# Performance work log

Measured on AMD Instinct MI355X. Metric: run time of the kernel, lower is better.

## Reference

```python
import jax, jax.numpy as jnp
import numpy as np

EMB, HEADS = 1024, 16
HD = EMB // HEADS


def setup_inputs() -> dict:
    key = jax.random.key(0)
    ks = jax.random.split(key, 9)
    B, T, C = 4, 2048, EMB
    s = 1.0 / np.sqrt(C)
    return {
        "x": jax.random.normal(ks[0], (B, T, C), jnp.float32),
        "Wq": jax.random.normal(ks[1], (C, C), jnp.float32) * s,
        "bq": jnp.zeros((C,), jnp.float32),
        "Wk": jax.random.normal(ks[2], (C, C), jnp.float32) * s,
        "bk": jnp.zeros((C,), jnp.float32),
        "Wv": jax.random.normal(ks[3], (C, C), jnp.float32) * s,
        "bv": jnp.zeros((C,), jnp.float32),
        "Wo": jax.random.normal(ks[4], (C, C), jnp.float32) * s,
        "bo": jnp.zeros((C,), jnp.float32),
    }


def _attn(x, Wq, bq, Wk, bk, Wv, bv, Wo, bo):
    B, T, C = x.shape
    # [B,T,C] -> [B,H,T,hd]
    def split(h):
        return h.reshape(B, T, HEADS, HD).transpose(0, 2, 1, 3)
    q = split(x @ Wq + bq)
    k = split(x @ Wk + bk)
    v = split(x @ Wv + bv)
    att = jnp.einsum("bhtd,bhsd->bhts", q, k) * (1.0 / np.sqrt(HD))
    causal = jnp.tril(jnp.ones((T, T), bool))  # [T,T]
    att = jnp.where(causal, att, -jnp.inf)
    att = jax.nn.softmax(att, axis=-1)
    y = jnp.einsum("bhts,bhsd->bhtd", att, v)
    y = y.transpose(0, 2, 1, 3).reshape(B, T, C)
    return y @ Wo + bo


def reference(x, Wq, bq, Wk, bk, Wv, bv, Wo, bo):
    return _attn(x, Wq, bq, Wk, bk, Wv, bv, Wo, bo)
```

## Files before the change

### kernel.cpp

```cpp
#include <hip/hip_runtime.h>
#include <cmath>

#define EMB 1024
#define HEADS 16
#define HD 64
#define BATCH 4
#define SEQ 2048
#define MTOT (BATCH * SEQ)

typedef __attribute__((ext_vector_type(8))) short short8;
typedef __attribute__((ext_vector_type(4))) float f32x4;
typedef __attribute__((ext_vector_type(16))) float f32x16;

__device__ __forceinline__ float b2f(unsigned short u) {
  union { unsigned int i; float f; } c; c.i = ((unsigned int)u) << 16; return c.f;
}
__device__ __forceinline__ unsigned short f2b(float f) {
  union { float f; unsigned int i; } c; c.f = f;
  unsigned int x = c.i;
  return (unsigned short)((x + 0x7fffu + ((x >> 16) & 1u)) >> 16);
}

#define GLD16(gp, lp) __builtin_amdgcn_global_load_lds( \
    (__attribute__((address_space(1))) unsigned int*)(gp), \
    (__attribute__((address_space(3))) unsigned int*)(lp), 16, 0, 0)

__global__ __launch_bounds__(256) void prep(
    const float* __restrict__ x, unsigned short* __restrict__ xb,
    const float* __restrict__ W0, const float* __restrict__ W1,
    const float* __restrict__ W2, const float* __restrict__ W3,
    unsigned short* __restrict__ Wt) {
  const int b = blockIdx.x;
  if (b < 4096) {
    const size_t i = ((size_t)b * 256 + threadIdx.x) * 8;
    const float4 a = *(const float4*)(x + i);
    const float4 c = *(const float4*)(x + i + 4);
    ushort4 lo = {f2b(a.x), f2b(a.y), f2b(a.z), f2b(a.w)};
    ushort4 hi = {f2b(c.x), f2b(c.y), f2b(c.z), f2b(c.w)};
    *(ushort4*)(xb + i) = lo;
    *(ushort4*)(xb + i + 4) = hi;
  } else {
    __shared__ float T[32][33];
    const int bb = b - 4096;
    const int z = bb >> 10;
    const float* W = (z == 0) ? W0 : (z == 1) ? W1 : (z == 2) ? W2 : W3;
    unsigned short* out = Wt + (size_t)z * EMB * EMB;
    const int k0 = (bb & 31) * 32, n0 = ((bb >> 5) & 31) * 32;
    const int tx = threadIdx.x & 31, ty = threadIdx.x >> 5;
#pragma unroll
    for (int r = 0; r < 4; ++r)
      T[ty + r * 8][tx] = W[(size_t)(k0 + ty + r * 8) * EMB + n0 + tx];
    __syncthreads();
#pragma unroll
    for (int r = 0; r < 4; ++r)
      out[(size_t)(n0 + ty + r * 8) * EMB + k0 + tx] = f2b(T[tx][ty + r * 8]);
  }
}

#define GEMM_STAGE64(Asrc_, Bsrc_, kb_)                                     \
  do {                                                                      \
    _Pragma("unroll")                                                       \
    for (int j_ = 0; j_ < 4; ++j_) {                                        \
      const int t_ = w * 4 + j_;                                            \
      const int r_ = t_ * 8 + r8;                                           \
      GLD16((Asrc_) + (size_t)(row0 + r_) * EMB + (kb_) + c8x,              \
            &As[t_ * 512]);                                                 \
      GLD16((Bsrc_) + (size_t)(col0 + r_) * EMB + (kb_) + c8x,              \
            &Bs[t_ * 512]);                                                 \
    }                                                                       \
  } while (0)

#define GEMM_KLOOP64(Asrc_, Bsrc_)                                          \
  const int r8 = lane >> 3;                                                 \
  const int c8x = ((lane & 7) ^ r8) * 8;                                    \
  for (int kb = 0; kb < EMB; kb += 64) {                                    \
    if (kb) __syncthreads();                                                \
    GEMM_STAGE64(Asrc_, Bsrc_, kb);                                         \
    __syncthreads();                                                        \
    _Pragma("unroll")                                                       \
    for (int kc = 0; kc < 2; ++kc) {                                        \
      short8 af[4], bf[4];                                                  \
      _Pragma("unroll")                                                     \
      for (int i = 0; i < 4; ++i)                                           \
        af[i] = *(const short8*)                                            \
            &As[(wm + i * 16 + m) * 64 + (((kc * 4 + g) ^ (m & 7)) * 8)];   \
      _Pragma("unroll")                                                     \
      for (int j = 0; j < 4; ++j)                                           \
        bf[j] = *(const short8*)                                            \
            &Bs[(wn + j * 16 + m) * 64 + (((kc * 4 + g) ^ (m & 7)) * 8)];   \
      _Pragma("unroll")                                                     \
      for (int i = 0; i < 4; ++i)                                           \
        _Pragma("unroll")                                                   \
        for (int j = 0; j < 4; ++j)                                         \
          acc[i][j] = __builtin_amdgcn_mfma_f32_16x16x32_bf16(              \
              af[i], bf[j], acc[i][j], 0, 0, 0);                            \
    }                                                                       \
  }

template <int OUTMODE>
__global__ __launch_bounds__(256) void gemm_mfma(
    const unsigned short* __restrict__ A, const unsigned short* __restrict__ Bt,
    const float* __restrict__ bias, void* __restrict__ outp) {
  __shared__ unsigned short As[128 * 64];
  __shared__ unsigned short Bs[128 * 64];
  const int tid = threadIdx.x;
  const int w = tid >> 6, lane = tid & 63;
  const int g = lane >> 4, m = lane & 15;
  const int row0 = blockIdx.x * 128, col0 = blockIdx.y * 128;
  const int wm = (w >> 1) * 64, wn = (w & 1) * 64;

  f32x4 acc[4][4];
#pragma unroll
  for (int i = 0; i < 4; ++i)
#pragma unroll
    for (int j = 0; j < 4; ++j) acc[i][j] = (f32x4){0.f, 0.f, 0.f, 0.f};

  GEMM_KLOOP64(A, Bt)

  float bv[4];
#pragma unroll
  for (int j = 0; j < 4; ++j) bv[j] = bias[col0 + wn + j * 16 + m];

#pragma unroll
  for (int i = 0; i < 4; ++i)
#pragma unroll
    for (int j = 0; j < 4; ++j)
#pragma unroll
      for (int r = 0; r < 4; ++r) {
        const size_t row = row0 + wm + i * 16 + g * 4 + r;
        const size_t col = col0 + wn + j * 16 + m;
        const float val = acc[i][j][r] + bv[j];
        if constexpr (OUTMODE == 0) ((float*)outp)[row * EMB + col] = val;
        else ((unsigned short*)outp)[row * EMB + col] = f2b(val);
      }
}

__global__ __launch_bounds__(256) void gemm_qkv(
    const unsigned short* __restrict__ A, const unsigned short* __restrict__ Wt,
    const float* __restrict__ b0, const float* __restrict__ b1,
    const float* __restrict__ b2, unsigned short* __restrict__ out) {
  __shared__ unsigned short As[128 * 64];
  __shared__ unsigned short Bs[128 * 64];
  const int z = blockIdx.z;
  const unsigned short* Bt = Wt + (size_t)z * EMB * EMB;
  const float* bias = (z == 0) ? b0 : ((z == 1) ? b1 : b2);
  const int tid = threadIdx.x;
  const int w = tid >> 6, lane = tid & 63;
  const int g = lane >> 4, m = lane & 15;
  const int row0 = blockIdx.x * 128, col0 = blockIdx.y * 128;
  const int wm = (w >> 1) * 64, wn = (w & 1) * 64;

  f32x4 acc[4][4];
#pragma unroll
  for (int i = 0; i < 4; ++i)
#pragma unroll
    for (int j = 0; j < 4; ++j) acc[i][j] = (f32x4){0.f, 0.f, 0.f, 0.f};

  GEMM_KLOOP64(A, Bt)

  float bv[4];
#pragma unroll
  for (int j = 0; j < 4; ++j) bv[j] = bias[col0 + wn + j * 16 + m];

  if (z == 2) {
    unsigned short* Vt = out + (size_t)2 * MTOT * EMB;
    const int bi = row0 >> 11;
    const int tb = (row0 & 2047) + wm;
#pragma unroll
    for (int i = 0; i < 4; ++i)
#pragma unroll
      for (int j = 0; j < 4; ++j) {
        const int col = col0 + wn + j * 16 + m;
        const int t0 = tb + i * 16 + g * 4;
        ushort4 pv = {f2b(acc[i][j][0] + bv[j]), f2b(acc[i][j][1] + bv[j]),
                      f2b(acc[i][j][2] + bv[j]), f2b(acc[i][j][3] + bv[j])};
        *(ushort4*)&Vt[(size_t)(bi * 1024 + col) * SEQ + t0] = pv;
      }
  } else {
    unsigned short* O = out + (size_t)z * MTOT * EMB;
#pragma unroll
    for (int i = 0; i < 4; ++i)
#pragma unroll
      for (int j = 0; j < 4; ++j)
#pragma unroll
        for (int r = 0; r < 4; ++r) {
          const size_t row = row0 + wm + i * 16 + g * 4 + r;
          const size_t col = col0 + wn + j * 16 + m;
          O[row * EMB + col] = f2b(acc[i][j][r] + bv[j]);
        }
  }
}

__global__ __launch_bounds__(256, 4) void flash_mfma(
    const unsigned short* __restrict__ Qg, const unsigned short* __restrict__ Kg,
    const unsigned short* __restrict__ Vtg, unsigned short* __restrict__ Yg) {
  __shared__ unsigned short Kl[2][64 * 64];
  __shared__ unsigned short Vl[2][64 * 64];
  const int tid = threadIdx.x;
  const int w = tid >> 6, lane = tid & 63;
  const int ql = lane & 31;
  const int hi = lane >> 5;

  const int gid = blockIdx.x;
  const int g2 = gid & 3;
  const int hb = (gid >> 2) & 63;
  const int g8 = gid >> 8;
  const int q4 = g2 * 4 + g8;
  const int qb = (q4 & 1) ? (q4 >> 1) : (15 - (q4 >> 1));
  const int bi = hb >> 4, hd = hb & 15;

  const size_t base = ((size_t)bi * SEQ) * EMB + (size_t)hd * HD;
  const size_t vtrow0 = (size_t)(bi * HEADS + hd) * HD;

  const int r8 = lane >> 3;
  const int c8 = ((lane & 7) ^ r8) * 8;

#define STAGE(tile_, buf_)                                                  \
  do {                                                                      \
    const int s0_ = (tile_) * 64;                                           \
    _Pragma("unroll")                                                       \
    for (int L = 0; L < 2; ++L) {                                           \
      const int rb_ = 16 * w + 8 * L;                                       \
      GLD16(Kg + base + (size_t)(s0_ + rb_ + r8) * EMB + c8,                \
            &Kl[buf_][rb_ * 64]);                                           \
    }                                                                       \
    _Pragma("unroll")                                                       \
    for (int L = 0; L < 2; ++L) {                                           \
      const int rb_ = 16 * w + 8 * L;                                       \
      GLD16(Vtg + (vtrow0 + rb_ + r8) * SEQ + s0_ + c8,                     \
            &Vl[buf_][rb_ * 64]);                                           \
    }                                                                       \
  } while (0)

  const int q0w = qb * 128 + 32 * w;
  const int q = q0w + ql;

  short8 qf[4];
#pragma unroll
  for (int s = 0; s < 4; ++s) {
    const uint4 u = *(const uint4*)(
        Qg + base + (size_t)q * EMB + s * 16 + hi * 8);
    const unsigned short* t = (const unsigned short*)&u;
    short8 qv;
#pragma unroll
    for (int j = 0; j < 8; ++j) qv[j] = (short)f2b(b2f(t[j]) * 0.18033688f);
    qf[s] = qv;
  }

  f32x16 acc[2];
#pragma unroll
  for (int db = 0; db < 2; ++db)
#pragma unroll
    for (int i = 0; i < 16; ++i) acc[db][i] = 0.f;
  float l_r = 0.f;

  const int nt = 2 * qb + 2;
  STAGE(0, 0);

  int buf = 0;
  for (int t = 0; t < nt; ++t) {
    asm volatile("s_waitcnt vmcnt(0)" ::: "memory");
    __builtin_amdgcn_s_barrier();
    if (t + 1 < nt) STAGE(t + 1, buf ^ 1);
    const int s0 = t * 64;
    if (s0 <= q0w + 31) {
      const unsigned short* K0 = Kl[buf];
      const unsigned short* V0 = Vl[buf];

      f32x16 sA[2];
      __builtin_amdgcn_s_setprio(1);
#pragma unroll
      for (int n = 0; n < 2; ++n) {
        const int row = 32 * n + ql;
        const int rb = row * 64, rk = row & 7;
        f32x16 z;
#pragma unroll
        for (int i = 0; i < 16; ++i) z[i] = 0.f;
#pragma unroll
        for (int s = 0; s < 4; ++s) {
          const short8 kf =
              *(const short8*)&K0[rb + (((2 * s + hi) ^ rk) * 8)];
          z = __builtin_amdgcn_mfma_f32_32x32x16_bf16(kf, qf[s], z, 0, 0, 0);
        }
        sA[n] = z;
      }
      __builtin_amdgcn_s_setprio(0);

      if (s0 + 63 > q) {
#pragma unroll
        for (int n = 0; n < 2; ++n)
#pragma unroll
          for (int r = 0; r < 16; ++r)
            if (s0 + 32 * n + (r & 3) + 8 * (r >> 2) + 4 * hi > q)
              sA[n][r] = -INFINITY;
      }

#pragma unroll
      for (int n = 0; n < 2; ++n)
#pragma unroll
        for (int r = 0; r < 16; ++r) {
          float p;
          asm("v_exp_f32 %0, %1" : "=v"(p) : "v"(sA[n][r]));
          sA[n][r] = p;
        }
      float s8[8];
#pragma unroll
      for (int i = 0; i < 8; ++i)
        s8[i] = (sA[0][2 * i] + sA[0][2 * i + 1]) +
                (sA[1][2 * i] + sA[1][2 * i + 1]);
      float ps = ((s8[0] + s8[1]) + (s8[2] + s8[3])) +
                 ((s8[4] + s8[5]) + (s8[6] + s8[7]));
      ps += __shfl_xor(ps, 32);
      l_r += ps;

      unsigned int pk[2][8];
#pragma unroll
      for (int n = 0; n < 2; ++n)
#pragma unroll
        for (int i = 0; i < 8; ++i) {
          unsigned int d;
          asm("v_cvt_pk_bf16_f32 %0, %1, %2"
              : "=v"(d) : "v"(sA[n][2 * i]), "v"(sA[n][2 * i + 1]));
          pk[n][i] = d;
        }
      union { unsigned int u[4]; short8 s; } pf[4];
#pragma unroll
      for (int ks = 0; ks < 4; ++ks) {
        const int n = ks >> 1, k4 = (ks & 1) * 4;
        unsigned int a0 = pk[n][k4 + 0], a1 = pk[n][k4 + 1];
        unsigned int b0 = pk[n][k4 + 2], b1 = pk[n][k4 + 3];
        asm("v_permlane32_swap_b32 %0, %1" : "+v"(a0), "+v"(b0));
        asm("v_permlane32_swap_b32 %0, %1" : "+v"(a1), "+v"(b1));
        pf[ks].u[0] = a0; pf[ks].u[1] = a1;
        pf[ks].u[2] = b0; pf[ks].u[3] = b1;
      }

      __builtin_amdgcn_s_setprio(1);
#pragma unroll
      for (int db = 0; db < 2; ++db) {
        const int row = 32 * db + ql;
        const int rb = row * 64, rk = row & 7;
#pragma unroll
        for (int ks = 0; ks < 4; ++ks) {
          const short8 vf =
              *(const short8*)&V0[rb + (((2 * ks + hi) ^ rk) * 8)];
          acc[db] = __builtin_amdgcn_mfma_f32_32x32x16_bf16(vf, pf[ks].s,
                                                            acc[db], 0, 0, 0);
        }
      }
      __builtin_amdgcn_s_setprio(0);
    }
    buf ^= 1;
  }

  const float iv = 1.f / l_r;
  unsigned short* Yrow = Yg + base + (size_t)q * EMB;
#pragma unroll
  for (int db = 0; db < 2; ++db)
#pragma unroll
    for (int r = 0; r < 16; r += 2) {
      unsigned int d;
      const float lo = acc[db][r] * iv, hh = acc[db][r + 1] * iv;
      asm("v_cvt_pk_bf16_f32 %0, %1, %2" : "=v"(d) : "v"(lo), "v"(hh));
      const int col = 32 * db + (r & 3) + 8 * (r >> 2) + 4 * hi;
      *(unsigned int*)(Yrow + col) = d;
    }
#undef STAGE
}

extern "C" void kernel_launch(void* const* d_in, const int* in_sizes, int n_in,
                              void* d_out, int out_size, void* d_ws, size_t ws_size,
                              hipStream_t stream) {
  const float* x  = (const float*)d_in[0];
  const float* Wq = (const float*)d_in[1];
  const float* bq = (const float*)d_in[2];
  const float* Wk = (const float*)d_in[3];
  const float* bk = (const float*)d_in[4];
  const float* Wv = (const float*)d_in[5];
  const float* bv = (const float*)d_in[6];
  const float* Wo = (const float*)d_in[7];
  const float* bo = (const float*)d_in[8];
  float* out = (float*)d_out;

  unsigned short* wqt = (unsigned short*)d_ws;
  unsigned short* wot = wqt + (size_t)3 * EMB * EMB;
  unsigned short* Q  = wqt + (size_t)4 * EMB * EMB;
  unsigned short* K  = Q + (size_t)MTOT * EMB;
  unsigned short* Vt = K + (size_t)MTOT * EMB;
  unsigned short* Y  = Vt + (size_t)MTOT * EMB;
  unsigned short* xb = Y + (size_t)MTOT * EMB;

  prep<<<dim3(8192), 256, 0, stream>>>(x, xb, Wq, Wk, Wv, Wo, wqt);

  gemm_qkv<<<dim3(MTOT / 128, EMB / 128, 3), 256, 0, stream>>>(
      xb, wqt, bq, bk, bv, Q);
  flash_mfma<<<dim3(1024), 256, 0, stream>>>(Q, K, Vt, Y);
  gemm_mfma<0><<<dim3(MTOT / 128, EMB / 128), 256, 0, stream>>>(
      Y, wot, bo, out);
}
```

Baseline: 142.3 us.

## Triple-buffer GEMM K-loop with 256x128 tiles and 512-thread blocks

Replaces the single-buffered 128x128 GEMM k-loop with a three-stage LDS ring that prefetches tile t+2 while computing tile t. Completion is tracked with explicit vmcnt waits and raw barriers instead of two __syncthreads per step. Blocks grow to 512 threads covering 256x128 output tiles, and the MFMA section is wrapped in s_setprio. The aim is to hide global-load latency and cut barrier stalls in the QKV and output projections, at the cost of about 144KB of LDS per block, which limits occupancy, and fewer blocks in the grid.

```diff
diff --git a/kernel.cpp b/kernel.cpp
--- a/kernel.cpp
+++ b/kernel.cpp
@@ -57,56 +57,75 @@
   }
 }
 
-#define GEMM_STAGE64(Asrc_, Bsrc_, kb_)                                     \
+#define TRI_STAGE_A(Asrc_, tt_, s_, p_)                                     \
+  GLD16((Asrc_) + (size_t)(row0 + (p_) * 64 + 8 * w + rs8) * EMB +          \
+            (tt_) * 64 + cs8,                                               \
+        &Al[s_][((p_) * 64 + 8 * w) * 64])
+#define TRI_STAGE_B(Bsrc_, tt_, s_, p_)                                     \
+  GLD16((Bsrc_) + (size_t)(col0 + (p_) * 64 + 8 * w + rs8) * EMB +          \
+            (tt_) * 64 + cs8,                                               \
+        &Bl[s_][((p_) * 64 + 8 * w) * 64])
+#define TRI_STAGE_TILE(Asrc_, Bsrc_, tt_, s_)                               \
   do {                                                                      \
-    _Pragma("unroll")                                                       \
-    for (int j_ = 0; j_ < 4; ++j_) {                                        \
-      const int t_ = w * 4 + j_;                                            \
-      const int r_ = t_ * 8 + r8;                                           \
-      GLD16((Asrc_) + (size_t)(row0 + r_) * EMB + (kb_) + c8x,              \
-            &As[t_ * 512]);                                                 \
-      GLD16((Bsrc_) + (size_t)(col0 + r_) * EMB + (kb_) + c8x,              \
-            &Bs[t_ * 512]);                                                 \
-    }                                                                       \
+    TRI_STAGE_A(Asrc_, tt_, s_, 0); TRI_STAGE_A(Asrc_, tt_, s_, 1);         \
+    TRI_STAGE_A(Asrc_, tt_, s_, 2); TRI_STAGE_A(Asrc_, tt_, s_, 3);         \
+    TRI_STAGE_B(Bsrc_, tt_, s_, 0); TRI_STAGE_B(Bsrc_, tt_, s_, 1);         \
   } while (0)
 
-#define GEMM_KLOOP64(Asrc_, Bsrc_)                                          \
-  const int r8 = lane >> 3;                                                 \
-  const int c8x = ((lane & 7) ^ r8) * 8;                                    \
-  for (int kb = 0; kb < EMB; kb += 64) {                                    \
-    if (kb) __syncthreads();                                                \
-    GEMM_STAGE64(Asrc_, Bsrc_, kb);                                         \
-    __syncthreads();                                                        \
+#define TRI_KLOOP(Asrc_, Bsrc_)                                             \
+  const int rs8 = lane >> 3;                                                \
+  const int cs8 = ((lane & 7) ^ rs8) * 8;                                   \
+  TRI_STAGE_TILE(Asrc_, Bsrc_, 0, 0);                                       \
+  TRI_STAGE_TILE(Asrc_, Bsrc_, 1, 1);                                       \
+  asm volatile("s_waitcnt vmcnt(6)" ::: "memory");                          \
+  __builtin_amdgcn_s_barrier();                                             \
+  for (int t = 0; t < 16; ++t) {                                            \
+    const int sc = t % 3, sn = (t + 2) % 3;                                 \
     _Pragma("unroll")                                                       \
     for (int kc = 0; kc < 2; ++kc) {                                        \
+      if (t + 2 < 16) {                                                     \
+        if (kc == 0) {                                                      \
+          TRI_STAGE_A(Asrc_, t + 2, sn, 0);                                 \
+          TRI_STAGE_A(Asrc_, t + 2, sn, 1);                                 \
+          TRI_STAGE_A(Asrc_, t + 2, sn, 2);                                 \
+        } else {                                                            \
+          TRI_STAGE_A(Asrc_, t + 2, sn, 3);                                 \
+          TRI_STAGE_B(Bsrc_, t + 2, sn, 0);                                 \
+          TRI_STAGE_B(Bsrc_, t + 2, sn, 1);                                 \
+        }                                                                   \
+      }                                                                     \
       short8 af[4], bf[4];                                                  \
       _Pragma("unroll")                                                     \
       for (int i = 0; i < 4; ++i)                                           \
-        af[i] = *(const short8*)                                            \
-            &As[(wm + i * 16 + m) * 64 + (((kc * 4 + g) ^ (m & 7)) * 8)];   \
+        af[i] = *(const short8*)&Al[sc][(wm + i * 16 + m) * 64 +            \
+                                        (((kc * 4 + g) ^ (m & 7)) * 8)];    \
       _Pragma("unroll")                                                     \
       for (int j = 0; j < 4; ++j)                                           \
-        bf[j] = *(const short8*)                                            \
-            &Bs[(wn + j * 16 + m) * 64 + (((kc * 4 + g) ^ (m & 7)) * 8)];   \
+        bf[j] = *(const short8*)&Bl[sc][(wn + j * 16 + m) * 64 +            \
+                                        (((kc * 4 + g) ^ (m & 7)) * 8)];    \
+      __builtin_amdgcn_s_setprio(1);                                        \
       _Pragma("unroll")                                                     \
       for (int i = 0; i < 4; ++i)                                           \
         _Pragma("unroll")                                                   \
         for (int j = 0; j < 4; ++j)                                         \
           acc[i][j] = __builtin_amdgcn_mfma_f32_16x16x32_bf16(              \
               af[i], bf[j], acc[i][j], 0, 0, 0);                            \
+      __builtin_amdgcn_s_setprio(0);                                        \
     }                                                                       \
+    if (t < 14) asm volatile("s_waitcnt vmcnt(6)" ::: "memory");            \
+    else if (t == 14) asm volatile("s_waitcnt vmcnt(0)" ::: "memory");      \
+    if (t < 15) __builtin_amdgcn_s_barrier();                               \
   }
 
-template <int OUTMODE>
-__global__ __launch_bounds__(256) void gemm_mfma(
+__global__ __launch_bounds__(512, 2) void gemm_tri(
     const unsigned short* __restrict__ A, const unsigned short* __restrict__ Bt,
-    const float* __restrict__ bias, void* __restrict__ outp) {
-  __shared__ unsigned short As[128 * 64];
-  __shared__ unsigned short Bs[128 * 64];
+    const float* __restrict__ bias, float* __restrict__ outp) {
+  __shared__ unsigned short Al[3][256 * 64];
+  __shared__ unsigned short Bl[3][128 * 64];
   const int tid = threadIdx.x;
   const int w = tid >> 6, lane = tid & 63;
   const int g = lane >> 4, m = lane & 15;
-  const int row0 = blockIdx.x * 128, col0 = blockIdx.y * 128;
+  const int row0 = blockIdx.x * 256, col0 = blockIdx.y * 128;
   const int wm = (w >> 1) * 64, wn = (w & 1) * 64;
 
   f32x4 acc[4][4];
@@ -115,7 +134,7 @@
 #pragma unroll
     for (int j = 0; j < 4; ++j) acc[i][j] = (f32x4){0.f, 0.f, 0.f, 0.f};
 
-  GEMM_KLOOP64(A, Bt)
+  TRI_KLOOP(A, Bt)
 
   float bv[4];
 #pragma unroll
@@ -129,25 +148,23 @@
       for (int r = 0; r < 4; ++r) {
         const size_t row = row0 + wm + i * 16 + g * 4 + r;
         const size_t col = col0 + wn + j * 16 + m;
-        const float val = acc[i][j][r] + bv[j];
-        if constexpr (OUTMODE == 0) ((float*)outp)[row * EMB + col] = val;
-        else ((unsigned short*)outp)[row * EMB + col] = f2b(val);
-      }
-}
-
-__global__ __launch_bounds__(256) void gemm_qkv(
+        outp[row * EMB + col] = acc[i][j][r] + bv[j];
+      }
+}
+
+__global__ __launch_bounds__(512, 2) void gemm_tri_qkv(
     const unsigned short* __restrict__ A, const unsigned short* __restrict__ Wt,
     const float* __restrict__ b0, const float* __restrict__ b1,
     const float* __restrict__ b2, unsigned short* __restrict__ out) {
-  __shared__ unsigned short As[128 * 64];
-  __shared__ unsigned short Bs[128 * 64];
+  __shared__ unsigned short Al[3][256 * 64];
+  __shared__ unsigned short Bl[3][128 * 64];
   const int z = blockIdx.z;
   const unsigned short* Bt = Wt + (size_t)z * EMB * EMB;
   const float* bias = (z == 0) ? b0 : ((z == 1) ? b1 : b2);
   const int tid = threadIdx.x;
   const int w = tid >> 6, lane = tid & 63;
   const int g = lane >> 4, m = lane & 15;
-  const int row0 = blockIdx.x * 128, col0 = blockIdx.y * 128;
+  const int row0 = blockIdx.x * 256, col0 = blockIdx.y * 128;
   const int wm = (w >> 1) * 64, wn = (w & 1) * 64;
 
   f32x4 acc[4][4];
@@ -156,7 +173,7 @@
 #pragma unroll
     for (int j = 0; j < 4; ++j) acc[i][j] = (f32x4){0.f, 0.f, 0.f, 0.f};
 
-  GEMM_KLOOP64(A, Bt)
+  TRI_KLOOP(A, Bt)
 
   float bv[4];
 #pragma unroll
@@ -392,9 +409,9 @@
 
   prep<<<dim3(8192), 256, 0, stream>>>(x, xb, Wq, Wk, Wv, Wo, wqt);
 
-  gemm_qkv<<<dim3(MTOT / 128, EMB / 128, 3), 256, 0, stream>>>(
+  gemm_tri_qkv<<<dim3(MTOT / 256, EMB / 128, 3), 512, 0, stream>>>(
       xb, wqt, bq, bk, bv, Q);
   flash_mfma<<<dim3(1024), 256, 0, stream>>>(Q, K, Vt, Y);
-  gemm_mfma<0><<<dim3(MTOT / 128, EMB / 128), 256, 0, stream>>>(
+  gemm_tri<<<dim3(MTOT / 256, EMB / 128), 512, 0, stream>>>(
       Y, wot, bo, out);
 }
```

After: 168.1 us. 18.1% more time.
